# Kernel tuning notes

Hardware: AMD Instinct MI355X
Metric: run time of the kernel (lower is better)

The kernel has to match this reference:

```python
import jax, jax.numpy as jnp
import numpy as np

GAMMA = 0.95        # gamma_lemma: persistence decay per cycle (eq. 12.1)
KAPPA = 0.1         # kappa_interfere: lateral interference strength (eq. 12.3)
T_STEPS = 50        # t_lemma_steps: integration window before selection (eq. 12.2)
FLOOR = 1e-6        # confidence_floor for peak-to-average ratio

B, N_CONCEPTS, N_LEMMAS = 4096, 1024, 512


def setup_inputs() -> dict:
    key = jax.random.key(0)
    k1, k2 = jax.random.split(key, 2)
    # kernel boundary hands in a normalized concept distribution
    c_raw = jax.random.uniform(k1, (B, N_CONCEPTS), dtype=jnp.float32)
    c_lex = c_raw / jnp.sum(c_raw, axis=-1, keepdims=True)
    # TiedSubstrate W_C_to_L: (out_dim=n_lemmas, in_dim=n_concepts)
    W = jax.random.normal(k2, (N_LEMMAS, N_CONCEPTS), dtype=jnp.float32) / np.sqrt(N_CONCEPTS)
    # persistent lemma activation buffer a_lemma, zero at reset
    a0 = jnp.zeros((B, N_LEMMAS), dtype=jnp.float32)
    return {"c_lex": c_lex, "W": W, "a0": a0}


def reference(c_lex, W, a0):
    """Integrate lemma activations for T_STEPS cycles, then select.

    Per cycle (eq. 12.1 + 12.3):
      a <- gamma * a + c_lex @ W^T            # decay + concept->lemma drive
      a <- a - kappa * (sum_j a_j - a)        # lateral interference from other lemmas
      a <- max(a, 0)                          # rectify activations
    Selection (eq. 12.2): argmax over lemmas; confidence = peak / max(mean, floor).
    """
    def step(a, _):
        a = GAMMA * a + jnp.einsum('bc,lc->bl', c_lex, W)   # (B, n_lemmas)
        a = a - KAPPA * (jnp.sum(a, axis=-1, keepdims=True) - a)
        a = jnp.maximum(a, 0.0)
        return a, None

    a, _ = jax.lax.scan(step, a0, None, length=T_STEPS)
    peak = jnp.max(a, axis=-1)
    mean = jnp.mean(a, axis=-1)
    confidence = peak / jnp.maximum(mean, FLOOR)
    selected = jnp.argmax(a, axis=-1)
    return a, selected, confidence
```

## Files before the change

kernel.cpp:

```cpp
#include <hip/hip_runtime.h>
#include <hip/hip_bf16.h>

#define BATCH 4096
#define NC    1024
#define NL    512
#define TSTEPS 50
#define GAMMA_C 0.95f
#define KAPPA_C 0.1f
#define FLOOR_C 1e-6f

typedef __attribute__((ext_vector_type(8))) short short8;
typedef __attribute__((ext_vector_type(4))) float f32x4;

__device__ inline void split_bf16(float x, unsigned short& h, unsigned short& l) {
    unsigned u = __float_as_uint(x);
    unsigned rh = u + 0x7FFFu + ((u >> 16) & 1u);
    h = (unsigned short)(rh >> 16);
    float hf = __uint_as_float((unsigned)h << 16);
    float r = x - hf;
    unsigned v = __float_as_uint(r);
    unsigned rl = v + 0x7FFFu + ((v >> 16) & 1u);
    l = (unsigned short)(rl >> 16);
}

__global__ __launch_bounds__(256)
void convert_split(const float* __restrict__ A, const float* __restrict__ W,
                   unsigned short* __restrict__ Ahi, unsigned short* __restrict__ Alo,
                   unsigned short* __restrict__ Whi, unsigned short* __restrict__ Wlo) {
    const int chunk = blockIdx.x * 256 + threadIdx.x;
    const int fidx  = chunk * 4;
    const float* src;
    unsigned short *dh, *dl;
    if (fidx < BATCH * NC) {
        src = A + fidx; dh = Ahi + fidx; dl = Alo + fidx;
    } else {
        const int o = fidx - BATCH * NC;
        src = W + o; dh = Whi + o; dl = Wlo + o;
    }
    const float4 v = *(const float4*)src;
    ushort4 h4, l4;
    split_bf16(v.x, h4.x, l4.x);
    split_bf16(v.y, h4.y, l4.y);
    split_bf16(v.z, h4.z, l4.z);
    split_bf16(v.w, h4.w, l4.w);
    *(ushort4*)dh = h4;
    *(ushort4*)dl = l4;
}

__device__ __forceinline__ void gld_lds16(const void* g, void* l) {
    __builtin_amdgcn_global_load_lds(
        (const __attribute__((address_space(1))) unsigned int*)g,
        (__attribute__((address_space(3))) unsigned int*)l,
        16, 0, 0);
}

#define TM 128
#define TN 128
#define GK 32

__global__ __launch_bounds__(256)
void gemm_bf16x2(const unsigned short* __restrict__ Ahi, const unsigned short* __restrict__ Alo,
                 const unsigned short* __restrict__ Whi, const unsigned short* __restrict__ Wlo,
                 float* __restrict__ Dp, int kPerSplit) {
    __shared__ unsigned short AsH[TM * GK];
    __shared__ unsigned short AsL[TM * GK];
    __shared__ unsigned short BsH[TN * GK];
    __shared__ unsigned short BsL[TN * GK];

    const int tid = threadIdx.x;
    const int m0 = blockIdx.x * TM;
    const int n0 = blockIdx.y * TN;
    const int kb = blockIdx.z * kPerSplit;

    const int lane = tid & 63;
    const int w    = tid >> 6;

    const int lr = lane >> 2;
    const int lk = (lane & 3) * 8;

    const int mw   = (w >> 1) * 64;
    const int nw   = (w & 1) * 64;
    const int sr   = lane & 15;
    const int quad = lane >> 4;

    const unsigned short* rAh = AsH + (mw + sr) * GK + quad * 8;
    const unsigned short* rAl = AsL + (mw + sr) * GK + quad * 8;
    const unsigned short* rBh = BsH + (nw + sr) * GK + quad * 8;
    const unsigned short* rBl = BsL + (nw + sr) * GK + quad * 8;

    f32x4 acc[4][4];
    #pragma unroll
    for (int i = 0; i < 4; ++i)
        #pragma unroll
        for (int j = 0; j < 4; ++j)
            acc[i][j] = (f32x4){0.f, 0.f, 0.f, 0.f};

    for (int kt = 0; kt < kPerSplit; kt += GK) {
        __syncthreads();
        const size_t ko = (size_t)(kb + kt);
        #pragma unroll
        for (int j = 0; j < 2; ++j) {
            const int i16 = w * 2 + j;
            const size_t ga = (size_t)(m0 + i16 * 16 + lr) * NC + ko + lk;
            const size_t gb = (size_t)(n0 + i16 * 16 + lr) * NC + ko + lk;
            gld_lds16(Ahi + ga, AsH + i16 * 512);
            gld_lds16(Alo + ga, AsL + i16 * 512);
            gld_lds16(Whi + gb, BsH + i16 * 512);
            gld_lds16(Wlo + gb, BsL + i16 * 512);
        }
        __syncthreads();

        short8 afh[4], afl[4], bfh[4], bfl[4];
        #pragma unroll
        for (int mi = 0; mi < 4; ++mi) {
            afh[mi] = *(const short8*)(rAh + mi * 16 * GK);
            afl[mi] = *(const short8*)(rAl + mi * 16 * GK);
        }
        #pragma unroll
        for (int ni = 0; ni < 4; ++ni) {
            bfh[ni] = *(const short8*)(rBh + ni * 16 * GK);
            bfl[ni] = *(const short8*)(rBl + ni * 16 * GK);
        }

        #pragma unroll
        for (int mi = 0; mi < 4; ++mi) {
            #pragma unroll
            for (int ni = 0; ni < 4; ++ni) {
                acc[mi][ni] = __builtin_amdgcn_mfma_f32_16x16x32_bf16(
                    afh[mi], bfh[ni], acc[mi][ni], 0, 0, 0);
                acc[mi][ni] = __builtin_amdgcn_mfma_f32_16x16x32_bf16(
                    afh[mi], bfl[ni], acc[mi][ni], 0, 0, 0);
                acc[mi][ni] = __builtin_amdgcn_mfma_f32_16x16x32_bf16(
                    afl[mi], bfh[ni], acc[mi][ni], 0, 0, 0);
            }
        }
    }

    float* Dz = Dp + (size_t)blockIdx.z * BATCH * NL;
    #pragma unroll
    for (int mi = 0; mi < 4; ++mi) {
        #pragma unroll
        for (int ni = 0; ni < 4; ++ni) {
            const int col = n0 + nw + ni * 16 + sr;
            #pragma unroll
            for (int r = 0; r < 4; ++r) {
                const int row = m0 + mw + mi * 16 + quad * 4 + r;
                Dz[(size_t)row * NL + col] = acc[mi][ni][r];
            }
        }
    }
}

template<int SK>
__global__ __launch_bounds__(256)
void iterate_select(const float* __restrict__ Dp,
                    float* __restrict__ a_out,
                    float* __restrict__ sel_out, float* __restrict__ conf_out) {
    const int lane = threadIdx.x & 63;
    const int wave = threadIdx.x >> 6;
    const int row  = blockIdx.x * 4 + wave;

    float d[8];
    {
        const float4* p0 = (const float4*)(Dp + (size_t)row * NL + lane * 8);
        float4 v0 = p0[0], v1 = p0[1];
        d[0] = v0.x; d[1] = v0.y; d[2] = v0.z; d[3] = v0.w;
        d[4] = v1.x; d[5] = v1.y; d[6] = v1.z; d[7] = v1.w;
        #pragma unroll
        for (int s = 1; s < SK; ++s) {
            const float4* ps = (const float4*)(Dp + (size_t)s * BATCH * NL
                                               + (size_t)row * NL + lane * 8);
            const float4 w0 = ps[0], w1 = ps[1];
            d[0] += w0.x; d[1] += w0.y; d[2] += w0.z; d[3] += w0.w;
            d[4] += w1.x; d[5] += w1.y; d[6] += w1.z; d[7] += w1.w;
        }
    }

    float a[8];
    #pragma unroll
    for (int j = 0; j < 8; ++j) a[j] = 0.f;

    const float K1 = 1.0f + KAPPA_C;

    for (int t = 0; t < TSTEPS; ++t) {
        #pragma unroll
        for (int j = 0; j < 8; ++j) a[j] = fmaf(GAMMA_C, a[j], d[j]);

        float t4a = a[0] + a[4], t4b = a[1] + a[5], t4c = a[2] + a[6], t4d = a[3] + a[7];
        float t2a = t4a + t4c, t2b = t4b + t4d;
        float S = t2a + t2b;

        S += __shfl_xor(S, 1, 64);
        S += __shfl_xor(S, 2, 64);
        S += __shfl_xor(S, 4, 64);
        S += __shfl_xor(S, 8, 64);
        S += __shfl_xor(S, 16, 64);
        S += __shfl_xor(S, 32, 64);

        const float h = -KAPPA_C * S;
        #pragma unroll
        for (int j = 0; j < 8; ++j) {
            const float v = fmaf(K1, a[j], h);
            a[j] = v > 0.f ? v : 0.f;
        }
    }

    float m4a = fmaxf(a[0], a[4]), m4b = fmaxf(a[1], a[5]);
    float m4c = fmaxf(a[2], a[6]), m4d = fmaxf(a[3], a[7]);
    float peak = fmaxf(fmaxf(m4a, m4b), fmaxf(m4c, m4d));
    float s4a = a[0] + a[4], s4b = a[1] + a[5], s4c = a[2] + a[6], s4d = a[3] + a[7];
    float ssum = (s4a + s4b) + (s4c + s4d);

    #pragma unroll
    for (int m = 1; m < 64; m <<= 1) {
        peak = fmaxf(peak, __shfl_xor(peak, m, 64));
        ssum += __shfl_xor(ssum, m, 64);
    }

    const float mean = ssum * (1.0f / (float)NL);
    const float conf = peak / fmaxf(mean, FLOOR_C);

    int idx = 0x7fffffff;
    #pragma unroll
    for (int j = 0; j < 8; ++j)
        if (a[j] == peak) idx = min(idx, lane * 8 + j);
    #pragma unroll
    for (int m = 1; m < 64; m <<= 1)
        idx = min(idx, __shfl_xor(idx, m, 64));

    float4* ar = (float4*)(a_out + (size_t)row * NL + lane * 8);
    float4 o0, o1;
    o0.x = a[0]; o0.y = a[1]; o0.z = a[2]; o0.w = a[3];
    o1.x = a[4]; o1.y = a[5]; o1.z = a[6]; o1.w = a[7];
    ar[0] = o0; ar[1] = o1;

    if (lane == 0) {
        if (sel_out)  sel_out[row]  = (float)idx;
        if (conf_out) conf_out[row] = conf;
    }
}

extern "C" void kernel_launch(void* const* d_in, const int* in_sizes, int n_in,
                              void* d_out, int out_size, void* d_ws, size_t ws_size,
                              hipStream_t stream) {
    const float* c_lex = (const float*)d_in[0];
    const float* W     = (const float*)d_in[1];

    float* D = (float*)d_ws;
    unsigned short* Ahi = (unsigned short*)(D + 2ull * BATCH * NL);
    unsigned short* Alo = Ahi + (size_t)BATCH * NC;
    unsigned short* Whi = Alo + (size_t)BATCH * NC;
    unsigned short* Wlo = Whi + (size_t)NL * NC;

    float* a_out = (float*)d_out;
    float* sel   = nullptr;
    float* conf  = nullptr;
    const int base = BATCH * NL;
    if (out_size >= base + 2 * BATCH) {
        sel  = a_out + base;
        conf = a_out + base + BATCH;
    } else if (out_size >= base + BATCH) {
        conf = a_out + base;
    }

    convert_split<<<dim3(4608), 256, 0, stream>>>(c_lex, W, Ahi, Alo, Whi, Wlo);

    const int kPerSplit = NC / 2;
    gemm_bf16x2<<<dim3(BATCH / TM, NL / TN, 2), 256, 0, stream>>>(
        Ahi, Alo, Whi, Wlo, D, kPerSplit);

    iterate_select<2><<<dim3(BATCH / 4), 256, 0, stream>>>(D, a_out, sel, conf);
}
```

Baseline: 117.9 us.

## Double-buffer GEMM LDS tiles and raise split-K from 2 to 4

Double-buffers the LDS tiles in the split-bf16 GEMM so the global-to-LDS loads for the next K slice are issued before computing on the current one, cutting one barrier per iteration. It also doubles the split-K factor to 4, giving 512 blocks instead of 256 for better CU occupancy. The cost is twice the LDS per block (possibly lower occupancy), twice the fp32 partial-sum workspace, and more partial reads in the iteration kernel. The workspace offset is moved to fit the extra partials.

```diff
diff --git a/kernel.cpp b/kernel.cpp
--- a/kernel.cpp
+++ b/kernel.cpp
@@ -62,10 +62,10 @@
 void gemm_bf16x2(const unsigned short* __restrict__ Ahi, const unsigned short* __restrict__ Alo,
                  const unsigned short* __restrict__ Whi, const unsigned short* __restrict__ Wlo,
                  float* __restrict__ Dp, int kPerSplit) {
-    __shared__ unsigned short AsH[TM * GK];
-    __shared__ unsigned short AsL[TM * GK];
-    __shared__ unsigned short BsH[TN * GK];
-    __shared__ unsigned short BsL[TN * GK];
+    __shared__ unsigned short AsH[2][TM * GK];
+    __shared__ unsigned short AsL[2][TM * GK];
+    __shared__ unsigned short BsH[2][TN * GK];
+    __shared__ unsigned short BsL[2][TN * GK];
 
     const int tid = threadIdx.x;
     const int m0 = blockIdx.x * TM;
@@ -83,11 +83,6 @@
     const int sr   = lane & 15;
     const int quad = lane >> 4;
 
-    const unsigned short* rAh = AsH + (mw + sr) * GK + quad * 8;
-    const unsigned short* rAl = AsL + (mw + sr) * GK + quad * 8;
-    const unsigned short* rBh = BsH + (nw + sr) * GK + quad * 8;
-    const unsigned short* rBl = BsL + (nw + sr) * GK + quad * 8;
-
     f32x4 acc[4][4];
     #pragma unroll
     for (int i = 0; i < 4; ++i)
@@ -95,20 +90,34 @@
         for (int j = 0; j < 4; ++j)
             acc[i][j] = (f32x4){0.f, 0.f, 0.f, 0.f};
 
-    for (int kt = 0; kt < kPerSplit; kt += GK) {
-        __syncthreads();
-        const size_t ko = (size_t)(kb + kt);
-        #pragma unroll
-        for (int j = 0; j < 2; ++j) {
-            const int i16 = w * 2 + j;
-            const size_t ga = (size_t)(m0 + i16 * 16 + lr) * NC + ko + lk;
-            const size_t gb = (size_t)(n0 + i16 * 16 + lr) * NC + ko + lk;
-            gld_lds16(Ahi + ga, AsH + i16 * 512);
-            gld_lds16(Alo + ga, AsL + i16 * 512);
-            gld_lds16(Whi + gb, BsH + i16 * 512);
-            gld_lds16(Wlo + gb, BsL + i16 * 512);
-        }
-        __syncthreads();
+    #define ISSUE_STAGE(ko, buf)                                                  \
+        {                                                                         \
+            _Pragma("unroll")                                                     \
+            for (int j = 0; j < 2; ++j) {                                         \
+                const int i16 = w * 2 + j;                                        \
+                const size_t ga = (size_t)(m0 + i16 * 16 + lr) * NC + (ko) + lk;  \
+                const size_t gb = (size_t)(n0 + i16 * 16 + lr) * NC + (ko) + lk;  \
+                gld_lds16(Ahi + ga, &AsH[buf][i16 * 512]);                        \
+                gld_lds16(Alo + ga, &AsL[buf][i16 * 512]);                        \
+                gld_lds16(Whi + gb, &BsH[buf][i16 * 512]);                        \
+                gld_lds16(Wlo + gb, &BsL[buf][i16 * 512]);                        \
+            }                                                                     \
+        }
+
+    const int nst = kPerSplit / GK;
+
+    ISSUE_STAGE(kb, 0);
+    __syncthreads();
+
+    for (int s = 0; s < nst; ++s) {
+        const int cur = s & 1;
+        if (s + 1 < nst)
+            ISSUE_STAGE(kb + (s + 1) * GK, cur ^ 1);
+
+        const unsigned short* rAh = &AsH[cur][(mw + sr) * GK + quad * 8];
+        const unsigned short* rAl = &AsL[cur][(mw + sr) * GK + quad * 8];
+        const unsigned short* rBh = &BsH[cur][(nw + sr) * GK + quad * 8];
+        const unsigned short* rBl = &BsL[cur][(nw + sr) * GK + quad * 8];
 
         short8 afh[4], afl[4], bfh[4], bfl[4];
         #pragma unroll
@@ -134,6 +143,8 @@
                     afl[mi], bfh[ni], acc[mi][ni], 0, 0, 0);
             }
         }
+
+        __syncthreads();
     }
 
     float* Dz = Dp + (size_t)blockIdx.z * BATCH * NL;
@@ -247,7 +258,7 @@
     const float* W     = (const float*)d_in[1];
 
     float* D = (float*)d_ws;
-    unsigned short* Ahi = (unsigned short*)(D + 2ull * BATCH * NL);
+    unsigned short* Ahi = (unsigned short*)(D + 4ull * BATCH * NL);
     unsigned short* Alo = Ahi + (size_t)BATCH * NC;
     unsigned short* Whi = Alo + (size_t)BATCH * NC;
     unsigned short* Wlo = Whi + (size_t)NL * NC;
@@ -265,9 +276,9 @@
 
     convert_split<<<dim3(4608), 256, 0, stream>>>(c_lex, W, Ahi, Alo, Whi, Wlo);
 
-    const int kPerSplit = NC / 2;
-    gemm_bf16x2<<<dim3(BATCH / TM, NL / TN, 2), 256, 0, stream>>>(
+    const int kPerSplit = NC / 4;
+    gemm_bf16x2<<<dim3(BATCH / TM, NL / TN, 4), 256, 0, stream>>>(
         Ahi, Alo, Whi, Wlo, D, kPerSplit);
 
-    iterate_select<2><<<dim3(BATCH / 4), 256, 0, stream>>>(D, a_out, sel, conf);
-}
+    iterate_select<4><<<dim3(BATCH / 4), 256, 0, stream>>>(D, a_out, sel, conf);
+}
```

Result: faster. 114.3 us (-3.0%).
